# Optimization experiments

Measured on AMD Instinct MI355X. Metric: run time of the kernel, lower is better.

Reference implementation:

```python
import jax, jax.numpy as jnp
import numpy as np

BATCH, SEQ, INPUT, HIDDEN, CLASSES = 256, 64, 512, 1024, 1000


def setup_inputs() -> dict:
    key = jax.random.key(0)
    ks = jax.random.split(key, 10)
    stdv = 1.0 / np.sqrt(HIDDEN)
    u = lambda k, shape: jax.random.uniform(k, shape, jnp.float32, -stdv, stdv)
    return {
        "x": jax.random.normal(ks[0], (BATCH, SEQ, INPUT), jnp.float32),
        # layer 1: gates ordered [i, f, g, o] along last dim
        "W1": u(ks[1], (INPUT, 4 * HIDDEN)),
        "U1": u(ks[2], (HIDDEN, 4 * HIDDEN)),
        "b1": u(ks[3], (4 * HIDDEN,)),
        # layer 2
        "W2": u(ks[4], (HIDDEN, 4 * HIDDEN)),
        "U2": u(ks[5], (HIDDEN, 4 * HIDDEN)),
        "b2": u(ks[6], (4 * HIDDEN,)),
        # output projection
        "Wo": u(ks[7], (HIDDEN, CLASSES)),
        "bo": u(ks[8], (CLASSES,)),
    }


def _lstm_cell(x, h, c, W, U, b):
    # gates: [B, 4H] -> i, f, g, o
    z = x @ W + h @ U + b
    i, f, g, o = jnp.split(z, 4, axis=-1)
    c_new = jax.nn.sigmoid(f) * c + jax.nn.sigmoid(i) * jnp.tanh(g)
    h_new = jax.nn.sigmoid(o) * jnp.tanh(c_new)
    return h_new, c_new


def reference(x, W1, U1, b1, W2, U2, b2, Wo, bo):
    B, H = x.shape[0], W1.shape[1] // 4
    xs = jnp.transpose(x, (1, 0, 2))  # [S, B, I]
    h0 = jnp.zeros((B, H), x.dtype)

    def step(carry, x_t):
        h1, c1, h2, c2 = carry
        h1, c1 = _lstm_cell(x_t, h1, c1, W1, U1, b1)
        h2, c2 = _lstm_cell(h1, h2, c2, W2, U2, b2)
        return (h1, c1, h2, c2), None

    (h1, c1, h2, c2), _ = jax.lax.scan(step, (h0, h0, h0, h0), xs)
    return h2 @ Wo + bo
```

## Files before the change

kernel.cpp:

```cpp
#include <hip/hip_runtime.h>
#include <hip/hip_bf16.h>

typedef __hip_bfloat16 bf16;
typedef short v8s __attribute__((ext_vector_type(8)));
typedef float v4f __attribute__((ext_vector_type(4)));
typedef unsigned long long u64;

#define BATCH 256
#define SEQ 64
#define INPUT 512
#define HIDDEN 1024
#define CLASSES 1000


__global__ __launch_bounds__(256) void conv_x(const float* __restrict__ x,
                                              bf16* __restrict__ Xf) {
    int gid = blockIdx.x * 256 + threadIdx.x;
    int lane = gid & 63;
    int k32 = (gid >> 6) & 15;
    int m16 = (gid >> 10) & 15;
    int tt  = gid >> 14;
    int row = lane & 15, quad = lane >> 4;
    int b_ = m16 * 16 + row;
    int k  = k32 * 32 + quad * 8;
    const float* src = x + ((size_t)(b_ * SEQ + tt) * INPUT + k);
    float4 v0 = *(const float4*)src;
    float4 v1 = *(const float4*)(src + 4);
    bf16 o[8] = {__float2bfloat16(v0.x), __float2bfloat16(v0.y),
                 __float2bfloat16(v0.z), __float2bfloat16(v0.w),
                 __float2bfloat16(v1.x), __float2bfloat16(v1.y),
                 __float2bfloat16(v1.z), __float2bfloat16(v1.w)};
    bf16* dst = Xf + (size_t)(tt * 256 + m16 * 16 + k32) * 512 + lane * 8;
    *(v8s*)dst = *(v8s*)o;
}

__global__ __launch_bounds__(256) void build_bf(const float* __restrict__ W,
                                                const float* __restrict__ U,
                                                int K0, int NT,
                                                bf16* __restrict__ dst) {
    __shared__ float tile[64][17];
    const int kt = blockIdx.x, hb = blockIdx.y, n16l = blockIdx.z;
    const int k0 = kt * 64;
    const int tid = threadIdx.x;
#pragma unroll
    for (int i = 0; i < 4; i++) {
        int idx = tid + i * 256;
        int c = idx & 15, kl = idx >> 4;
        int k = k0 + kl;
        int srccol = (n16l * 2 + (c >> 3)) * 1024 + hb * 8 + (c & 7);
        float v = (k < K0) ? W[(size_t)k * 4096 + srccol]
                           : U[(size_t)(k - K0) * 4096 + srccol];
        tile[kl][c] = v;
    }
    __syncthreads();
    if (tid < 128) {
        int k32l = tid >> 6, l = tid & 63;
        bf16 o[8];
#pragma unroll
        for (int j = 0; j < 8; j++)
            o[j] = __float2bfloat16(tile[k32l * 32 + (l >> 4) * 8 + j][l & 15]);
        *(v8s*)(dst + ((size_t)(hb * 2 + n16l) * NT + kt * 2 + k32l) * 512 + l * 8) = *(v8s*)o;
    }
}

__global__ __launch_bounds__(256) void build_wof(const float* __restrict__ Wo,
                                                 bf16* __restrict__ dst) {
    __shared__ float tile[64][17];
    const int h16 = blockIdx.y, kt = blockIdx.x;
    const int k0 = kt * 64, nb = h16 * 16;
    const int tid = threadIdx.x;
#pragma unroll
    for (int i = 0; i < 4; i++) {
        int idx = tid + i * 256;
        int kl = idx >> 4, c = idx & 15;
        int k = k0 + kl;
        float v = (nb + c < CLASSES) ? Wo[(size_t)k * CLASSES + nb + c] : 0.f;
        tile[kl][c] = v;
    }
    __syncthreads();
    if (tid < 128) {
        int k32l = tid >> 6, l = tid & 63;
        int col = l & 15, quad = l >> 4;
        bf16 o[8];
#pragma unroll
        for (int j = 0; j < 8; j++)
            o[j] = __float2bfloat16(tile[k32l * 32 + quad * 8 + j][col]);
        int k32 = kt * 2 + k32l;
        *(v8s*)(dst + (size_t)(h16 * 32 + k32) * 512 + l * 8) = *(v8s*)o;
    }
}

__device__ __forceinline__ void spinwait(const int* p, int target) {
    while (__hip_atomic_load(p, __ATOMIC_RELAXED, __HIP_MEMORY_SCOPE_AGENT) < target)
        __builtin_amdgcn_s_sleep(1);
}

template<int NT, int NA>
__device__ __forceinline__ void run_layer(
    const bf16* __restrict__ A0all, size_t A0stride,
    bf16* __restrict__ hall,
    const bf16* __restrict__ hz,
    const bf16* __restrict__ Bl,
    bf16* __restrict__ hstage,
    const float* __restrict__ bias,
    int hb,
    const int* __restrict__ waitA,
    const int* __restrict__ waitSelf,
    int* __restrict__ pub)
{
    const size_t HB = (size_t)BATCH * HIDDEN;
    const int tid = threadIdx.x;
    const int lane = tid & 63, wave = tid >> 6;
    const int col = lane & 15, quad = lane >> 4;
    const bool hicol = (col & 8) != 0;
    const int K32 = hb >> 2, Q = hb & 3;

    const float bI = bias[0 * 1024 + hb * 8 + (col & 7)];
    const float bF = bias[1 * 1024 + hb * 8 + (col & 7)];
    const float bG = bias[2 * 1024 + hb * 8 + (col & 7)];
    const float bO = bias[3 * 1024 + hb * 8 + (col & 7)];

    float cc[4] = {0.f, 0.f, 0.f, 0.f};

    const bf16* bl0 = Bl + lane * 8;
    const bf16* bl1 = Bl + (size_t)NT * 512 + lane * 8;

    for (int t = 0; t < SEQ; t++) {
        if (tid == 0) {
            if (waitA) spinwait(waitA + t * 64, 128);
            if (t > 0) spinwait(waitSelf + (t - 1) * 64, 128);
        }
        __syncthreads();

        const bf16* A0 = A0all + (size_t)t * A0stride;
        const bf16* A1 = t ? (hall + (size_t)(t - 1) * HB) : hz;
        const bf16* ax0 = A0 + (size_t)((wave * 2 + 0) * NA) * 512 + lane * 8;
        const bf16* ax1 = A0 + (size_t)((wave * 2 + 1) * NA) * 512 + lane * 8;
        const bf16* ah0 = A1 + (size_t)((wave * 2 + 0) * 32) * 512 + lane * 8;
        const bf16* ah1 = A1 + (size_t)((wave * 2 + 1) * 32) * 512 + lane * 8;

        v4f acc[2][2] = {};
        v8s ra[8][2];
        v8s rb[4][2];

#define ISSUE_A(K, S) do {                                                        \
    const bf16* p0_ = ((K) < NA) ? (ax0 + (size_t)(K) * 512)                      \
                                 : (ah0 + (size_t)((K) - NA) * 512);              \
    const bf16* p1_ = ((K) < NA) ? (ax1 + (size_t)(K) * 512)                      \
                                 : (ah1 + (size_t)((K) - NA) * 512);              \
    asm volatile("global_load_dwordx4 %0, %1, off" : "=v"(ra[S][0]) : "v"(p0_));  \
    asm volatile("global_load_dwordx4 %0, %1, off" : "=v"(ra[S][1]) : "v"(p1_));  \
} while (0)
#define IB(K, S) do {                                                            \
    rb[S][0] = *(const v8s*)(bl0 + (size_t)(K) * 512);                           \
    rb[S][1] = *(const v8s*)(bl1 + (size_t)(K) * 512);                           \
} while (0)

#pragma unroll
        for (int k = 0; k < 8; k++) ISSUE_A(k, k);
#pragma unroll
        for (int k = 0; k < 4; k++) IB(k, k);

#pragma unroll
        for (int k = 0; k < NT; k++) {
            const int sa = k & 7, sb = k & 3;
            asm volatile("s_waitcnt vmcnt(%0)"
                         :: "n"(2 * ((NT - k) < 8 ? (NT - k) : 8) - 2));
            __builtin_amdgcn_sched_barrier(0);
            acc[0][0] = __builtin_amdgcn_mfma_f32_16x16x32_bf16(ra[sa][0], rb[sb][0], acc[0][0], 0, 0, 0);
            acc[0][1] = __builtin_amdgcn_mfma_f32_16x16x32_bf16(ra[sa][0], rb[sb][1], acc[0][1], 0, 0, 0);
            acc[1][0] = __builtin_amdgcn_mfma_f32_16x16x32_bf16(ra[sa][1], rb[sb][0], acc[1][0], 0, 0, 0);
            acc[1][1] = __builtin_amdgcn_mfma_f32_16x16x32_bf16(ra[sa][1], rb[sb][1], acc[1][1], 0, 0, 0);
            if (k + 8 < NT) ISSUE_A(k + 8, sa);
            if (k + 4 < NT) IB(k + 4, sb);
        }
#undef ISSUE_A
#undef IB

#pragma unroll
        for (int r = 0; r < 4; r++) {
            float send0 = hicol ? acc[0][0][r] : acc[1][0][r];
            float send1 = hicol ? acc[0][1][r] : acc[1][1][r];
            float recv0 = __shfl_xor(send0, 8, 64);
            float recv1 = __shfl_xor(send1, 8, 64);
            float own0 = hicol ? acc[1][0][r] : acc[0][0][r];
            float own1 = hicol ? acc[1][1][r] : acc[0][1][r];
            float zi = (hicol ? recv0 : own0) + bI;
            float zf = (hicol ? own0 : recv0) + bF;
            float zg = (hicol ? recv1 : own1) + bG;
            float zo = (hicol ? own1 : recv1) + bO;
            float ig = 1.f / (1.f + __expf(-zi));
            float fg = 1.f / (1.f + __expf(-zf));
            float e2g = __expf(2.f * zg);
            float gg = (e2g - 1.f) / (e2g + 1.f);
            float og = 1.f / (1.f + __expf(-zo));
            float cn = fg * cc[r] + ig * gg;
            float e2c = __expf(2.f * cn);
            float th = (e2c - 1.f) / (e2c + 1.f);
            cc[r] = cn;
            int m_local = wave * 32 + (hicol ? 16 : 0) + quad * 4 + r;
            hstage[m_local * 8 + (col & 7)] = __float2bfloat16(og * th);
        }

        if (lane < 32) {
            int row = wave * 32 + lane;
            v8s hv = *(const v8s*)(hstage + row * 8);
            bf16* houtt = hall + (size_t)t * HB;
            size_t eoff = ((size_t)(row >> 4) * 32 + K32) * 512
                        + (size_t)((row & 15) + 16 * Q) * 8;
            u64 qq[2];
            *(v8s*)qq = hv;
            u64* dp = (u64*)(houtt + eoff);
            __hip_atomic_store(dp,     qq[0], __ATOMIC_RELAXED, __HIP_MEMORY_SCOPE_AGENT);
            __hip_atomic_store(dp + 1, qq[1], __ATOMIC_RELAXED, __HIP_MEMORY_SCOPE_AGENT);
        }
        __syncthreads();

        if (tid == 0)
            __hip_atomic_fetch_add(pub + t * 64, 1,
                                   __ATOMIC_RELAXED, __HIP_MEMORY_SCOPE_AGENT);
    }
}

__global__ __launch_bounds__(512, 2) void lstm_persist(
    const bf16* __restrict__ Xf,
    const bf16* __restrict__ Bf1, const bf16* __restrict__ Bf2,
    const float* __restrict__ b1, const float* __restrict__ b2,
    bf16* __restrict__ h1all, bf16* __restrict__ h2all,
    const bf16* __restrict__ hz,
    int* __restrict__ flags1, int* __restrict__ flags2)
{
    extern __shared__ char smem[];
    bf16* Bl = (bf16*)smem;
    bf16* hstage = (bf16*)(smem + 131072);

    const int b = blockIdx.x;
    const int layer = b >> 7;
    const int hb = b & 127;
    const int tid = threadIdx.x;

    {
        const int NTl = layer ? 64 : 48;
        const bf16* Bsrc = (layer ? Bf2 : Bf1) + (size_t)(hb * 2 * NTl) * 512;
        const int nbytes = NTl * 2 * 1024;
        for (int o = tid * 16; o < nbytes; o += 512 * 16)
            *(uint4*)(smem + o) = *(const uint4*)((const char*)Bsrc + o);
    }
    __syncthreads();

    if (layer == 0)
        run_layer<48, 16>(Xf, (size_t)BATCH * INPUT, h1all, hz, Bl, hstage,
                          b1, hb, nullptr, flags1, flags1);
    else
        run_layer<64, 32>(h1all, (size_t)BATCH * HIDDEN, h2all, hz, Bl, hstage,
                          b2, hb, flags1, flags2, flags2);
}

__global__ __launch_bounds__(256, 2) void proj_kernel(
    const bf16* __restrict__ H,
    const bf16* __restrict__ Wof,
    const float* __restrict__ bo,
    float* __restrict__ Out)
{
    const int mblk = blockIdx.x, nblk = blockIdx.y;
    const int tid = threadIdx.x;
    const int lane = tid & 63;
    const int wave = tid >> 6;
    const int mw = wave >> 1, nw = wave & 1;
    const int col = lane & 15, quad = lane >> 4;

    const int m16 = mblk * 4 + mw * 2;
    const bf16* ah0 = H + (size_t)(m16 * 32) * 512 + lane * 8;
    const bf16* ah1 = H + (size_t)((m16 + 1) * 32) * 512 + lane * 8;
    const int n16a = nblk * 4 + nw * 2, n16b = n16a + 1;
    const bf16* bb0 = Wof + (size_t)(n16a * 32) * 512 + lane * 8;
    const bf16* bb1 = Wof + (size_t)(n16b * 32) * 512 + lane * 8;

    v4f acc00{}, acc01{}, acc10{}, acc11{};
    v8s ra0[8], ra1[8], rb0[8], rb1[8];

#define ISSUE(KK, SLOT) do {                          \
    const int kk_ = (KK);                             \
    ra0[SLOT] = *(const v8s*)(ah0 + kk_ * 512);       \
    ra1[SLOT] = *(const v8s*)(ah1 + kk_ * 512);       \
    rb0[SLOT] = *(const v8s*)(bb0 + kk_ * 512);       \
    rb1[SLOT] = *(const v8s*)(bb1 + kk_ * 512);       \
} while (0)

#pragma unroll
    for (int u = 0; u < 8; u++) ISSUE(u, u);

    for (int base = 0; base < 32; base += 8) {
#pragma unroll
        for (int u = 0; u < 8; u++) {
            acc00 = __builtin_amdgcn_mfma_f32_16x16x32_bf16(ra0[u], rb0[u], acc00, 0, 0, 0);
            acc01 = __builtin_amdgcn_mfma_f32_16x16x32_bf16(ra0[u], rb1[u], acc01, 0, 0, 0);
            acc10 = __builtin_amdgcn_mfma_f32_16x16x32_bf16(ra1[u], rb0[u], acc10, 0, 0, 0);
            acc11 = __builtin_amdgcn_mfma_f32_16x16x32_bf16(ra1[u], rb1[u], acc11, 0, 0, 0);
            const int k2 = base + u + 8;
            if (k2 < 32) ISSUE(k2, u);
        }
    }
#undef ISSUE

    const int n0 = n16a * 16 + col, n1 = n16b * 16 + col;
    const float bo0 = (n0 < CLASSES) ? bo[n0] : 0.f;
    const float bo1 = (n1 < CLASSES) ? bo[n1] : 0.f;
#pragma unroll
    for (int i = 0; i < 2; i++) {
        const int row = mblk * 64 + mw * 32 + i * 16 + quad * 4;
        v4f a0 = i ? acc10 : acc00;
        v4f a1 = i ? acc11 : acc01;
#pragma unroll
        for (int r = 0; r < 4; r++) {
            if (n0 < CLASSES) Out[(size_t)(row + r) * CLASSES + n0] = a0[r] + bo0;
            if (n1 < CLASSES) Out[(size_t)(row + r) * CLASSES + n1] = a1[r] + bo1;
        }
    }
}

extern "C" void kernel_launch(void* const* d_in, const int* in_sizes, int n_in,
                              void* d_out, int out_size, void* d_ws, size_t ws_size,
                              hipStream_t stream) {
    const float* x  = (const float*)d_in[0];
    const float* W1 = (const float*)d_in[1];
    const float* U1 = (const float*)d_in[2];
    const float* b1 = (const float*)d_in[3];
    const float* W2 = (const float*)d_in[4];
    const float* U2 = (const float*)d_in[5];
    const float* b2 = (const float*)d_in[6];
    const float* Wo = (const float*)d_in[7];
    const float* bo = (const float*)d_in[8];
    float* out = (float*)d_out;

    char* ws = (char*)d_ws;
    size_t off = 0;
    auto alloc = [&](size_t bytes) -> void* {
        void* p = ws + off;
        off += (bytes + 255) & ~(size_t)255;
        return p;
    };
    bf16* Xf    = (bf16*)alloc((size_t)SEQ * BATCH * INPUT * 2);
    bf16* Bf1   = (bf16*)alloc((size_t)128 * 2 * 48 * 512 * 2);
    bf16* Bf2   = (bf16*)alloc((size_t)128 * 2 * 64 * 512 * 2);
    bf16* Wof   = (bf16*)alloc((size_t)64 * 32 * 512 * 2);
    bf16* h1all = (bf16*)alloc((size_t)SEQ * BATCH * HIDDEN * 2);
    bf16* h2all = (bf16*)alloc((size_t)SEQ * BATCH * HIDDEN * 2);
    bf16* hz    = (bf16*)alloc((size_t)BATCH * HIDDEN * 2);
    int* flags1 = (int*)alloc(64 * 64 * 4);
    int* flags2 = (int*)alloc(64 * 64 * 4);

    hipMemsetAsync(hz, 0, (size_t)BATCH * HIDDEN * 2, stream);
    hipMemsetAsync(flags1, 0, 64 * 64 * 4, stream);
    hipMemsetAsync(flags2, 0, 64 * 64 * 4, stream);

    conv_x<<<4096, 256, 0, stream>>>(x, Xf);
    build_bf<<<dim3(24, 128, 2), 256, 0, stream>>>(W1, U1, 512, 48, Bf1);
    build_bf<<<dim3(32, 128, 2), 256, 0, stream>>>(W2, U2, 1024, 64, Bf2);
    build_wof<<<dim3(16, 64), 256, 0, stream>>>(Wo, Wof);

    lstm_persist<<<256, 512, 135168, stream>>>(Xf, Bf1, Bf2, b1, b2,
                                               h1all, h2all, hz, flags1, flags2);

    proj_kernel<<<dim3(4, 16), 256, 0, stream>>>(
        h2all + (size_t)(SEQ - 1) * BATCH * HIDDEN, Wof, bo, out);
}
```

Measured before the change: 970.2 us.

## Defer recurrent-state wait until input-projection MFMAs are issued

The wait on the previous timestep's hidden state is moved from the top of each step to the point in the K loop where the recurrent columns start. The input-projection loads and MFMAs (x for layer 0, h1 for layer 1) can then run while other blocks are still publishing h. The full __syncthreads is replaced with a bare s_barrier wrapped in scheduling fences, and the upstream-layer wait is kept separate. Without the memory fence that __syncthreads implied, there is some risk of reading stale hidden-state data.

```diff
diff --git a/kernel.cpp b/kernel.cpp
--- a/kernel.cpp
+++ b/kernel.cpp
@@ -95,7 +95,13 @@
         __builtin_amdgcn_s_sleep(1);
 }
 
-template<int NT, int NA>
+__device__ __forceinline__ void soft_barrier() {
+    __builtin_amdgcn_sched_barrier(0);
+    __builtin_amdgcn_s_barrier();
+    __builtin_amdgcn_sched_barrier(0);
+}
+
+template<int NT, int NA, int KSELF>
 __device__ __forceinline__ void run_layer(
     const bf16* __restrict__ A0all, size_t A0stride,
     bf16* __restrict__ hall,
@@ -126,12 +132,6 @@
     const bf16* bl1 = Bl + (size_t)NT * 512 + lane * 8;
 
     for (int t = 0; t < SEQ; t++) {
-        if (tid == 0) {
-            if (waitA) spinwait(waitA + t * 64, 128);
-            if (t > 0) spinwait(waitSelf + (t - 1) * 64, 128);
-        }
-        __syncthreads();
-
         const bf16* A0 = A0all + (size_t)t * A0stride;
         const bf16* A1 = t ? (hall + (size_t)(t - 1) * HB) : hz;
         const bf16* ax0 = A0 + (size_t)((wave * 2 + 0) * NA) * 512 + lane * 8;
@@ -139,11 +139,16 @@
         const bf16* ah0 = A1 + (size_t)((wave * 2 + 0) * 32) * 512 + lane * 8;
         const bf16* ah1 = A1 + (size_t)((wave * 2 + 1) * 32) * 512 + lane * 8;
 
+        if (waitA) {
+            if (tid == 0) spinwait(waitA + t * 64, 128);
+            soft_barrier();
+        }
+
         v4f acc[2][2] = {};
         v8s ra[8][2];
         v8s rb[4][2];
 
-#define ISSUE_A(K, S) do {                                                        \
+#define IA(K, S) do {                                                             \
     const bf16* p0_ = ((K) < NA) ? (ax0 + (size_t)(K) * 512)                      \
                                  : (ah0 + (size_t)((K) - NA) * 512);              \
     const bf16* p1_ = ((K) < NA) ? (ax1 + (size_t)(K) * 512)                      \
@@ -151,18 +156,24 @@
     asm volatile("global_load_dwordx4 %0, %1, off" : "=v"(ra[S][0]) : "v"(p0_));  \
     asm volatile("global_load_dwordx4 %0, %1, off" : "=v"(ra[S][1]) : "v"(p1_));  \
 } while (0)
-#define IB(K, S) do {                                                            \
-    rb[S][0] = *(const v8s*)(bl0 + (size_t)(K) * 512);                           \
-    rb[S][1] = *(const v8s*)(bl1 + (size_t)(K) * 512);                           \
+#define IB(K, S) do {                                                             \
+    rb[S][0] = *(const v8s*)(bl0 + (size_t)(K) * 512);                            \
+    rb[S][1] = *(const v8s*)(bl1 + (size_t)(K) * 512);                            \
 } while (0)
 
 #pragma unroll
-        for (int k = 0; k < 8; k++) ISSUE_A(k, k);
+        for (int k = 0; k < 8; k++) IA(k, k);
 #pragma unroll
         for (int k = 0; k < 4; k++) IB(k, k);
 
 #pragma unroll
         for (int k = 0; k < NT; k++) {
+            if (k == KSELF) {
+                if (t) {
+                    if (tid == 0) spinwait(waitSelf + (t - 1) * 64, 128);
+                    soft_barrier();
+                }
+            }
             const int sa = k & 7, sb = k & 3;
             asm volatile("s_waitcnt vmcnt(%0)"
                          :: "n"(2 * ((NT - k) < 8 ? (NT - k) : 8) - 2));
@@ -171,10 +182,10 @@
             acc[0][1] = __builtin_amdgcn_mfma_f32_16x16x32_bf16(ra[sa][0], rb[sb][1], acc[0][1], 0, 0, 0);
             acc[1][0] = __builtin_amdgcn_mfma_f32_16x16x32_bf16(ra[sa][1], rb[sb][0], acc[1][0], 0, 0, 0);
             acc[1][1] = __builtin_amdgcn_mfma_f32_16x16x32_bf16(ra[sa][1], rb[sb][1], acc[1][1], 0, 0, 0);
-            if (k + 8 < NT) ISSUE_A(k + 8, sa);
+            if (k + 8 < NT) IA(k + 8, sa);
             if (k + 4 < NT) IB(k + 4, sb);
         }
-#undef ISSUE_A
+#undef IA
 #undef IB
 
 #pragma unroll
@@ -249,11 +260,11 @@
     __syncthreads();
 
     if (layer == 0)
-        run_layer<48, 16>(Xf, (size_t)BATCH * INPUT, h1all, hz, Bl, hstage,
-                          b1, hb, nullptr, flags1, flags1);
+        run_layer<48, 16, 8>(Xf, (size_t)BATCH * INPUT, h1all, hz, Bl, hstage,
+                             b1, hb, nullptr, flags1, flags1);
     else
-        run_layer<64, 32>(h1all, (size_t)BATCH * HIDDEN, h2all, hz, Bl, hstage,
-                          b2, hb, flags1, flags2, flags2);
+        run_layer<64, 32, 24>(h1all, (size_t)BATCH * HIDDEN, h2all, hz, Bl, hstage,
+                              b2, hb, flags1, flags2, flags2);
 }
 
 __global__ __launch_bounds__(256, 2) void proj_kernel(
```

Result: faster. 845.7 us (-12.8%).
